# Optimization experiments

Measured on AMD Instinct MI355X. Metric: run time of the kernel, lower is better.

The kernel has to match this reference:

```python
import jax, jax.numpy as jnp
import numpy as np
from jax import lax

NB, HH, WW, C = 8, 64, 64, 192
G, K, DW_K, PA_K = 12, 3, 5, 3
GC, P = C // G, K * K
PAD, STRIDE, DIL = 1, 1, 1
OFFSET_SCALE = 1.0
LN_EPS = 1e-5


def _grid_sample(img, grid):
    # img: (B,Cc,H,W); grid: (B,L,P,2) xy in [-1,1]; bilinear, zeros padding, align_corners=False
    B, Cc, H, W = img.shape
    gx = (grid[..., 0] + 1.0) * (W * 0.5) - 0.5
    gy = (grid[..., 1] + 1.0) * (H * 0.5) - 0.5
    x0, y0 = jnp.floor(gx), jnp.floor(gy)

    def gather(xi, yi):
        valid = (xi >= 0) & (xi <= W - 1) & (yi >= 0) & (yi <= H - 1)
        xc = jnp.clip(xi, 0, W - 1).astype(jnp.int32)
        yc = jnp.clip(yi, 0, H - 1).astype(jnp.int32)
        v = jax.vmap(lambda im, y, x: im[:, y, x])(img, yc, xc)  # (B,Cc,L,P)
        return v * valid[:, None].astype(img.dtype)

    wx1, wy1 = gx - x0, gy - y0
    wx0, wy0 = 1.0 - wx1, 1.0 - wy1
    return (gather(x0, y0) * (wx0 * wy0)[:, None]
            + gather(x0 + 1.0, y0) * (wx1 * wy0)[:, None]
            + gather(x0, y0 + 1.0) * (wx0 * wy1)[:, None]
            + gather(x0 + 1.0, y0 + 1.0) * (wx1 * wy1)[:, None])


def _dcnv3_core(x, offset, mask):
    # x: (N,H,W,C) projected input; offset: (N,H,W,G*P*2); mask: (N,H,W,G*P)
    N, H, W, _ = x.shape
    xp = jnp.pad(x, ((0, 0), (PAD, PAD), (PAD, PAD), (0, 0)))
    Hp, Wp = H + 2 * PAD, W + 2 * PAD
    Ho, Wo = offset.shape[1], offset.shape[2]
    base = (DIL * (K - 1)) // 2 + 0.5
    ref_y = (base + jnp.arange(Ho) * STRIDE) / Hp
    ref_x = (base + jnp.arange(Wo) * STRIDE) / Wp
    ref = jnp.stack(jnp.broadcast_arrays(ref_x[None, :], ref_y[:, None]), -1)  # (Ho,Wo,2) xy
    start = -((DIL * (K - 1)) // 2)
    pts = (start + jnp.arange(K) * DIL).astype(x.dtype)
    gxg = jnp.broadcast_to((pts / Wp)[:, None], (K, K))  # w offset varies along dim0 (torch order)
    gyg = jnp.broadcast_to((pts / Hp)[None, :], (K, K))
    grid = jnp.tile(jnp.stack([gxg, gyg], -1).reshape(P, 2), (G, 1))  # (G*P,2)
    loc = ref[None, :, :, None, :] + grid * OFFSET_SCALE  # (1,Ho,Wo,G*P,2)
    norm = jnp.array([Wp, Hp], dtype=x.dtype)
    loc = loc + offset.reshape(N, Ho, Wo, G * P, 2) * OFFSET_SCALE / norm
    sg = 2.0 * loc - 1.0  # (N,Ho,Wo,G*P,2)
    img = xp.reshape(N, Hp * Wp, G, GC).transpose(0, 2, 3, 1).reshape(N * G, GC, Hp, Wp)
    grd = sg.reshape(N, Ho * Wo, G, P, 2).transpose(0, 2, 1, 3, 4).reshape(N * G, Ho * Wo, P, 2)
    samp = _grid_sample(img, grd)  # (N*G, GC, L, P)
    m = mask.reshape(N, Ho * Wo, G, P).transpose(0, 2, 1, 3).reshape(N * G, 1, Ho * Wo, P)
    out = (samp * m).sum(-1)  # (N*G, GC, L)
    return out.reshape(N, G, GC, Ho * Wo).transpose(0, 3, 1, 2).reshape(N, Ho, Wo, C)


def _dcnv3(x, dw_w, dw_b, ln_g, ln_b, off_w, off_b, msk_w, msk_b, in_w, in_b, out_w, out_b, cfs_w, cfs_b):
    N, H, W, _ = x.shape
    x_proj = x @ in_w + in_b
    # depthwise conv (5x5) -> LayerNorm (channels_last) -> GELU(exact)
    u = lax.conv_general_dilated(x, dw_w, (1, 1), 'SAME',
                                 dimension_numbers=('NHWC', 'HWIO', 'NHWC'),
                                 feature_group_count=C) + dw_b
    mu = u.mean(-1, keepdims=True)
    var = ((u - mu) ** 2).mean(-1, keepdims=True)
    u = (u - mu) * lax.rsqrt(var + LN_EPS) * ln_g + ln_b
    u = jax.nn.gelu(u, approximate=False)
    offset = u @ off_w + off_b  # (N,H,W,G*P*2)
    m = jax.nn.softmax((u @ msk_w + msk_b).reshape(N, H, W, G, P), axis=-1).reshape(N, H, W, G * P)
    y = _dcnv3_core(x_proj, offset, m)
    cfs = jax.nn.sigmoid(u @ cfs_w + cfs_b)  # (N,H,W,G)
    cfs = jnp.repeat(cfs, GC, axis=-1)       # (N,H,W,C), group-blockwise
    y = y * (1.0 - cfs) + x_proj * cfs
    return y @ out_w + out_b


def _patch_attention(x):
    # x: (N,H,W,C) -> std over softmax'd 3x3 neighbor scores: (N,H,W)
    N, H, W, _ = x.shape
    pad = (PA_K - 1) // 2
    xp = jnp.pad(x, ((0, 0), (pad, pad), (pad, pad), (0, 0)))
    neigh = jnp.stack([xp[:, i:i + H, j:j + W, :] for i in range(PA_K) for j in range(PA_K)],
                      axis=-1)  # (N,H,W,C,K1*K2), torch unfold ordering
    scores = jnp.einsum('nhwc,nhwck->nhwk', x, neigh)
    sm = jax.nn.softmax(scores, axis=-1)
    return jnp.std(sm, axis=-1, ddof=1)  # torch.std is unbiased


def setup_inputs() -> dict:
    key = jax.random.key(0)
    ks = jax.random.split(key, 8)
    s = 0.02
    return {
        'x': jax.random.normal(ks[0], (NB, HH, WW, C), jnp.float32),
        'dw_w': jax.random.normal(ks[1], (DW_K, DW_K, 1, C), jnp.float32) * s,
        'dw_b': jnp.zeros((C,), jnp.float32),
        'ln_g': jnp.ones((C,), jnp.float32),
        'ln_b': jnp.zeros((C,), jnp.float32),
        'off_w': jax.random.normal(ks[2], (C, G * P * 2), jnp.float32) * s,
        'off_b': jnp.zeros((G * P * 2,), jnp.float32),
        'msk_w': jax.random.normal(ks[3], (C, G * P), jnp.float32) * s,
        'msk_b': jnp.zeros((G * P,), jnp.float32),
        'in_w': jax.random.normal(ks[4], (C, C), jnp.float32) * s,
        'in_b': jnp.zeros((C,), jnp.float32),
        'out_w': jax.random.normal(ks[5], (C, C), jnp.float32) * s,
        'out_b': jnp.zeros((C,), jnp.float32),
        'cfs_w': jax.random.normal(ks[6], (C, G), jnp.float32) * s,
        'cfs_b': jnp.zeros((G,), jnp.float32),
    }


def reference(x, dw_w, dw_b, ln_g, ln_b, off_w, off_b, msk_w, msk_b, in_w, in_b, out_w, out_b, cfs_w, cfs_b):
    x1 = _dcnv3(x, dw_w, dw_b, ln_g, ln_b, off_w, off_b, msk_w, msk_b, in_w, in_b, out_w, out_b, cfs_w, cfs_b)
    mask = _patch_attention(x1)           # (N,H,W)
    return x + x1 * mask[..., None]
```

## Files before the change

### kernel.cpp

```cpp
#include <hip/hip_runtime.h>
#include <hip/hip_bf16.h>
#include <math.h>

#define NB 8
#define HH 64
#define WW 64
#define C 192
#define G 12
#define GC 16
#define P 9
#define NPIX (NB*HH*WW)

typedef __attribute__((ext_vector_type(8))) short short8;
typedef __attribute__((ext_vector_type(4))) float f32x4;
typedef unsigned short ushort;

__device__ __forceinline__ ushort to_bf16(float f) {
  __hip_bfloat16 b = __float2bfloat16(f);
  return *(ushort*)&b;
}
__device__ __forceinline__ float bf2f(ushort u) {
  union { unsigned u; float f; } cv; cv.u = ((unsigned)u) << 16; return cv.f;
}
__device__ __forceinline__ float bflo(unsigned u) {
  union { unsigned v; float f; } c; c.v = u << 16; return c.f;
}
__device__ __forceinline__ float bfhi(unsigned u) {
  union { unsigned v; float f; } c; c.v = u & 0xffff0000u; return c.f;
}

__global__ __launch_bounds__(256) void cvt_kernel(const float* __restrict__ in,
                                                  ushort* __restrict__ out) {
  int i = blockIdx.x*256 + threadIdx.x;
  float4 v0 = ((const float4*)in)[2*i];
  float4 v1 = ((const float4*)in)[2*i+1];
  short8 r;
  r[0]=to_bf16(v0.x); r[1]=to_bf16(v0.y); r[2]=to_bf16(v0.z); r[3]=to_bf16(v0.w);
  r[4]=to_bf16(v1.x); r[5]=to_bf16(v1.y); r[6]=to_bf16(v1.z); r[7]=to_bf16(v1.w);
  ((short8*)out)[i] = r;
}

__global__ void prep_w_kernel(const float* __restrict__ in_w, const float* __restrict__ out_w,
    const float* __restrict__ off_w, const float* __restrict__ msk_w, const float* __restrict__ cfs_w,
    const float* __restrict__ off_b, const float* __restrict__ msk_b, const float* __restrict__ cfs_b,
    ushort* __restrict__ in_wt, ushort* __restrict__ out_wt, ushort* __restrict__ wf_t,
    float* __restrict__ bf_bias) {
  int idx = blockIdx.x*256 + threadIdx.x;
  if (idx < 36864) {
    int n = idx/192, k = idx%192;
    in_wt[idx] = to_bf16(in_w[k*192 + n]);
  } else if (idx < 73728) {
    int j = idx - 36864; int n = j/192, k = j%192;
    out_wt[j] = to_bf16(out_w[k*192 + n]);
  } else if (idx < 147456) {
    int j = idx - 73728; int n = j/192, k = j%192;
    float v = 0.f;
    if (n < 216)      v = off_w[k*216 + n];
    else if (n < 324) v = msk_w[k*108 + (n-216)];
    else if (n < 336) v = cfs_w[k*12  + (n-324)];
    wf_t[j] = to_bf16(v);
  }
  if (idx < 384) {
    float b = 0.f;
    if (idx < 216)      b = off_b[idx];
    else if (idx < 324) b = msk_b[idx-216];
    else if (idx < 336) b = cfs_b[idx-324];
    bf_bias[idx] = b;
  }
}

template<int NW, int NSTORE, bool BF16OUT>
__global__ __launch_bounds__(256) void mfma_gemm(const ushort* __restrict__ A,
    const ushort* __restrict__ Wt, const float* __restrict__ bias,
    void* __restrict__ Cout_) {
  __shared__ ushort As[4*128*8];
  __shared__ ushort Bs[4*64*8];
  int pix0 = blockIdx.x * 128, n0 = blockIdx.y * 64;
  int tid = threadIdx.x;
  int wid = tid >> 6, lane = tid & 63;
  int lr = lane >> 4, lc = lane & 15;

  f32x4 acc[2][4];
  #pragma unroll
  for (int m=0;m<2;m++)
    #pragma unroll
    for (int j=0;j<4;j++) acc[m][j] = (f32x4){0.f,0.f,0.f,0.f};

  int sa0_kb = tid >> 7,        sa0_row = tid & 127;
  int sa1_kb = (tid+256) >> 7,  sa1_row = (tid+256) & 127;
  int sb_kb  = tid >> 6,        sb_n    = tid & 63;

  short8 pa0, pa1, pb;
  auto load_tile = [&](int k0) {
    pa0 = *(const short8*)&A[(size_t)(pix0 + sa0_row)*192 + k0 + sa0_kb*8];
    pa1 = *(const short8*)&A[(size_t)(pix0 + sa1_row)*192 + k0 + sa1_kb*8];
    pb  = *(const short8*)&Wt[(size_t)(n0 + sb_n)*192 + k0 + sb_kb*8];
  };
  load_tile(0);

  for (int t = 0; t < 6; t++) {
    __syncthreads();
    *(short8*)&As[(size_t)tid*8]        = pa0;
    *(short8*)&As[(size_t)(tid+256)*8]  = pa1;
    *(short8*)&Bs[(size_t)tid*8]        = pb;
    __syncthreads();
    if (t < 5) load_tile((t+1)*32);
    short8 a0 = *(const short8*)&As[(size_t)(lr*128 + wid*32 + lc)*8];
    short8 a1 = *(const short8*)&As[(size_t)(lr*128 + wid*32 + 16 + lc)*8];
    #pragma unroll
    for (int j=0;j<4;j++) {
      short8 b = *(const short8*)&Bs[(size_t)(lr*64 + j*16 + lc)*8];
      acc[0][j] = __builtin_amdgcn_mfma_f32_16x16x32_bf16(a0, b, acc[0][j], 0,0,0);
      acc[1][j] = __builtin_amdgcn_mfma_f32_16x16x32_bf16(a1, b, acc[1][j], 0,0,0);
    }
  }
  #pragma unroll
  for (int j=0;j<4;j++) {
    int col = n0 + j*16 + lc;
    if (NW != NSTORE && col >= NSTORE) continue;
    float bb = bias[col];
    #pragma unroll
    for (int m=0;m<2;m++) {
      size_t rbase = pix0 + wid*32 + m*16 + lr*4;
      #pragma unroll
      for (int r=0;r<4;r++) {
        float v = acc[m][j][r] + bb;
        if (BF16OUT) ((ushort*)Cout_)[(rbase + r)*NSTORE + col] = to_bf16(v);
        else         ((float*) Cout_)[(rbase + r)*NSTORE + col] = v;
      }
    }
  }
}

#define SEG 16
__global__ __launch_bounds__(192) void dw_ln_gelu_kernel(const float* __restrict__ x,
    const float* __restrict__ dw_w, const float* __restrict__ dw_b,
    const float* __restrict__ ln_g, const float* __restrict__ ln_b,
    ushort* __restrict__ u_out) {
  int blk = blockIdx.x;
  int qw = blk & 3; int nh = blk >> 2;
  int h = nh & 63, n = nh >> 6;
  int c = threadIdx.x;
  int w0 = qw * SEG;

  float kw[25];
  #pragma unroll
  for (int t=0;t<25;t++) kw[t] = dw_w[t*C + c];

  float acc[SEG];
  float bb = dw_b[c];
  #pragma unroll
  for (int i=0;i<SEG;i++) acc[i] = bb;

  #pragma unroll
  for (int i=0;i<5;i++) {
    int hy = h + i - 2;
    if (hy < 0 || hy >= HH) continue;
    const float* rowp = &x[(((size_t)n*HH + hy)*WW)*C + c];
    #pragma unroll
    for (int wi=0; wi<SEG+4; wi++) {
      int w_in = w0 - 2 + wi;
      if (w_in < 0 || w_in >= WW) continue;
      float v = rowp[(size_t)w_in*C];
      #pragma unroll
      for (int j=0;j<5;j++) {
        int a = wi - j;
        if (a >= 0 && a < SEG) acc[a] += v * kw[i*5+j];
      }
    }
  }

  __shared__ float lds_acc[SEG][C+1];
  __shared__ float part1[SEG][12], part2[SEG][12];
  __shared__ float mu_s[SEG], rs_s[SEG];
  #pragma unroll
  for (int i=0;i<SEG;i++) lds_acc[i][c] = acc[i];
  __syncthreads();
  {
    int p = threadIdx.x & 15, chunk = threadIdx.x >> 4;
    float s1 = 0.f, s2 = 0.f;
    #pragma unroll
    for (int k=0;k<16;k++) {
      float v = lds_acc[p][chunk*16 + k];
      s1 += v; s2 += v*v;
    }
    part1[p][chunk] = s1; part2[p][chunk] = s2;
  }
  __syncthreads();
  if (threadIdx.x < SEG) {
    int p = threadIdx.x;
    float t1 = 0.f, t2 = 0.f;
    #pragma unroll
    for (int k=0;k<12;k++){ t1 += part1[p][k]; t2 += part2[p][k]; }
    float mu = t1 * (1.0f/C);
    float var = t2 * (1.0f/C) - mu*mu;
    mu_s[p] = mu; rs_s[p] = rsqrtf(var + 1e-5f);
  }
  __syncthreads();
  float gg = ln_g[c], lb = ln_b[c];
  size_t obase = ((size_t)nh*WW + w0)*C + c;
  #pragma unroll
  for (int i=0;i<SEG;i++) {
    float uv = (acc[i] - mu_s[i])*rs_s[i]*gg + lb;
    uv = 0.5f*uv*(1.0f + erff(uv*0.70710678118654752f));
    u_out[obase + (size_t)i*C] = to_bf16(uv);
  }
}

#define SPX 4
__global__ __launch_bounds__(192) void sample_kernel(const float* __restrict__ omc,
    const ushort* __restrict__ x_proj, ushort* __restrict__ y_out) {
  int pix0 = blockIdx.x * SPX;
  int n = pix0 >> 12;
  int hw = pix0 & 4095; int h = hw >> 6; int w0 = hw & 63;
  int tid = threadIdx.x;
  __shared__ int   addrs[SPX*108*4];
  __shared__ float wts[SPX*108*4];
  __shared__ float msm[SPX][108];
  __shared__ float cfss[SPX][12];

  for (int i = tid; i < SPX*108; i += 192) {
    int px = i / 108, gp = i % 108;
    int p = gp % 9;
    const float pts[3] = {-1.f, 0.f, 1.f};
    float ox = omc[(size_t)(pix0+px)*336 + 2*gp];
    float oy = omc[(size_t)(pix0+px)*336 + 2*gp + 1];
    float gx = 1.0f + (float)(w0+px) + pts[p/3] + ox;
    float gy = 1.0f + (float)h + pts[p%3] + oy;
    float x0f = floorf(gx), y0f = floorf(gy);
    float wx1 = gx - x0f, wy1 = gy - y0f;
    float wx0 = 1.f-wx1, wy0 = 1.f-wy1;
    int x0 = (int)x0f, y0 = (int)y0f;
    bool xv0 = (x0   >= 1) && (x0   <= 64);
    bool xv1 = (x0+1 >= 1) && (x0+1 <= 64);
    bool yv0 = (y0   >= 1) && (y0   <= 64);
    bool yv1 = (y0+1 >= 1) && (y0+1 <= 64);
    int base = n*HH*WW*C;
    int4 a4;
    a4.x = (yv0&&xv0) ? (base + ((y0-1)*WW + (x0-1))*C)*2 : 0;
    a4.y = (yv0&&xv1) ? (base + ((y0-1)*WW + (x0  ))*C)*2 : 0;
    a4.z = (yv1&&xv0) ? (base + ((y0  )*WW + (x0-1))*C)*2 : 0;
    a4.w = (yv1&&xv1) ? (base + ((y0  )*WW + (x0  ))*C)*2 : 0;
    ((int4*)addrs)[i] = a4;
    float4 w4;
    w4.x = (yv0&&xv0) ? wx0*wy0 : 0.f;
    w4.y = (yv0&&xv1) ? wx1*wy0 : 0.f;
    w4.z = (yv1&&xv0) ? wx0*wy1 : 0.f;
    w4.w = (yv1&&xv1) ? wx1*wy1 : 0.f;
    ((float4*)wts)[i] = w4;
  }
  if (tid < SPX*12) {
    int px = tid / 12, gg = tid % 12;
    const float* mrow = &omc[(size_t)(pix0+px)*336 + 216 + gg*9];
    float m = -1e30f;
    #pragma unroll
    for (int p=0;p<P;p++) m = fmaxf(m, mrow[p]);
    float e[P]; float s = 0.f;
    #pragma unroll
    for (int p=0;p<P;p++){ e[p] = expf(mrow[p]-m); s += e[p]; }
    float inv = 1.0f/s;
    #pragma unroll
    for (int p=0;p<P;p++) msm[px][gg*9+p] = e[p]*inv;
  } else if (tid < SPX*12*2) {
    int q = tid - SPX*12;
    int px = q / 12, gg = q % 12;
    cfss[px][gg] = 1.0f/(1.0f+expf(-omc[(size_t)(pix0+px)*336 + 324 + gg]));
  }
  __syncthreads();
  for (int i = tid; i < SPX*108; i += 192) {
    int px = i / 108, gp = i % 108;
    float m = msm[px][gp] * (1.0f - cfss[px][gp/9]);
    f32x4 w4 = *(f32x4*)&wts[i*4];
    w4 *= m;
    *(f32x4*)&wts[i*4] = w4;
  }
  __syncthreads();
  int px = tid / 48, s = tid % 48;
  int g = s >> 2;
  int cb = s * 8;
  const char* xb = (const char*)x_proj;
  float4 accY = {0.f,0.f,0.f,0.f};
  #pragma unroll
  for (int p=0;p<P;p++){
    int gp = g*P + p;
    int4   a4 = ((const int4*)addrs)[px*108+gp];
    float4 w4 = ((const float4*)wts)[px*108+gp];
    uint2 q0 = *(const uint2*)(xb + (unsigned)(a4.x + cb));
    uint2 q1 = *(const uint2*)(xb + (unsigned)(a4.y + cb));
    uint2 q2 = *(const uint2*)(xb + (unsigned)(a4.z + cb));
    uint2 q3 = *(const uint2*)(xb + (unsigned)(a4.w + cb));
    accY.x += w4.x*bflo(q0.x) + w4.y*bflo(q1.x) + w4.z*bflo(q2.x) + w4.w*bflo(q3.x);
    accY.y += w4.x*bfhi(q0.x) + w4.y*bfhi(q1.x) + w4.z*bfhi(q2.x) + w4.w*bfhi(q3.x);
    accY.z += w4.x*bflo(q0.y) + w4.y*bflo(q1.y) + w4.z*bflo(q2.y) + w4.w*bflo(q3.y);
    accY.w += w4.x*bfhi(q0.y) + w4.y*bfhi(q1.y) + w4.z*bfhi(q2.y) + w4.w*bfhi(q3.y);
  }
  float cf = cfss[px][g];
  uint2 qx = *(const uint2*)(xb + ((size_t)(pix0+px)*C)*2 + cb);
  accY.x += bflo(qx.x)*cf;
  accY.y += bfhi(qx.x)*cf;
  accY.z += bflo(qx.y)*cf;
  accY.w += bfhi(qx.y)*cf;
  ushort4 r;
  r.x = to_bf16(accY.x); r.y = to_bf16(accY.y);
  r.z = to_bf16(accY.z); r.w = to_bf16(accY.w);
  *(ushort4*)&y_out[(size_t)(pix0+px)*C + s*4] = r;
}

__global__ __launch_bounds__(256) void pattn_kernel(const float* __restrict__ x,
    const ushort* __restrict__ x1, float* __restrict__ out) {
  int pix = blockIdx.x*4 + (threadIdx.x>>6);
  int lane = threadIdx.x & 63;
  int n = pix / (HH*WW); int hw = pix % (HH*WW); int h = hw / WW; int w = hw % WW;
  size_t base = (size_t)pix*C;
  float cen[3];
  #pragma unroll
  for (int q=0;q<3;q++) cen[q] = bf2f(x1[base + lane + 64*q]);
  float sc[9];
  #pragma unroll
  for (int i=0;i<3;i++){
    int hy = h+i-1;
    #pragma unroll
    for (int j=0;j<3;j++){
      int wx = w+j-1;
      float a = 0.f;
      if (hy>=0 && hy<HH && wx>=0 && wx<WW){
        size_t nb = ((size_t)(n*HH+hy)*WW + wx)*C;
        #pragma unroll
        for (int q=0;q<3;q++) a += cen[q]*bf2f(x1[nb + lane + 64*q]);
      }
      sc[i*3+j]=a;
    }
  }
  #pragma unroll
  for (int k=0;k<9;k++){
    #pragma unroll
    for (int o=32;o>0;o>>=1) sc[k] += __shfl_xor(sc[k], o);
  }
  float m = sc[0];
  #pragma unroll
  for (int k=1;k<9;k++) m = fmaxf(m, sc[k]);
  float pr[9]; float s = 0.f;
  #pragma unroll
  for (int k=0;k<9;k++){ pr[k] = expf(sc[k]-m); s += pr[k]; }
  float inv = 1.0f/s;
  float mean = 0.f;
  #pragma unroll
  for (int k=0;k<9;k++){ pr[k] *= inv; mean += pr[k]; }
  mean *= (1.0f/9.0f);
  float var = 0.f;
  #pragma unroll
  for (int k=0;k<9;k++){ float d = pr[k]-mean; var += d*d; }
  float sd = sqrtf(var*(1.0f/8.0f));
  #pragma unroll
  for (int q=0;q<3;q++){
    int c = lane + 64*q;
    out[base+c] = x[base+c] + bf2f(x1[base+c])*sd;
  }
}

extern "C" void kernel_launch(void* const* d_in, const int* in_sizes, int n_in,
                              void* d_out, int out_size, void* d_ws, size_t ws_size,
                              hipStream_t stream) {
  const float* x     = (const float*)d_in[0];
  const float* dw_w  = (const float*)d_in[1];
  const float* dw_b  = (const float*)d_in[2];
  const float* ln_g  = (const float*)d_in[3];
  const float* ln_b  = (const float*)d_in[4];
  const float* off_w = (const float*)d_in[5];
  const float* off_b = (const float*)d_in[6];
  const float* msk_w = (const float*)d_in[7];
  const float* msk_b = (const float*)d_in[8];
  const float* in_w  = (const float*)d_in[9];
  const float* in_b  = (const float*)d_in[10];
  const float* out_w = (const float*)d_in[11];
  const float* out_b = (const float*)d_in[12];
  const float* cfs_w = (const float*)d_in[13];
  const float* cfs_b = (const float*)d_in[14];
  float* outp = (float*)d_out;

  float*  omc    = (float*)d_ws;
  ushort* xproj  = (ushort*)(omc + (size_t)NPIX*336);
  ushort* x_bf   = xproj + (size_t)NPIX*192;
  ushort* u_bf   = x_bf + (size_t)NPIX*192;
  ushort* in_wt  = u_bf + (size_t)NPIX*192;
  ushort* out_wt = in_wt + 192*192;
  ushort* wf_t   = out_wt + 192*192;
  float*  bfb    = (float*)(wf_t + 384*192);

  cvt_kernel<<<NPIX*192/8/256, 256, 0, stream>>>(x, x_bf);
  prep_w_kernel<<<(147456+255)/256, 256, 0, stream>>>(in_w, out_w, off_w, msk_w, cfs_w,
                                                       off_b, msk_b, cfs_b,
                                                       in_wt, out_wt, wf_t, bfb);
  mfma_gemm<192,192,true><<<dim3(NPIX/128, 3), 256, 0, stream>>>(x_bf, in_wt, in_b, xproj);
  dw_ln_gelu_kernel<<<NB*HH*4, 192, 0, stream>>>(x, dw_w, dw_b, ln_g, ln_b, u_bf);
  mfma_gemm<384,336,false><<<dim3(NPIX/128, 6), 256, 0, stream>>>(u_bf, wf_t, bfb, omc);
  sample_kernel<<<NPIX/SPX, 192, 0, stream>>>(omc, xproj, u_bf);
  mfma_gemm<192,192,true><<<dim3(NPIX/128, 3), 256, 0, stream>>>(u_bf, out_wt, out_b, x_bf);
  pattn_kernel<<<NPIX/4, 256, 0, stream>>>(x, x_bf, outp);
}
```

Measured before the change: 157.8 us.

## Store offset/mask GEMM output in bf16, batch sample loads, tile patch attention in LDS

The offset/mask/cfs GEMM now writes bf16 instead of fp32, which halves the traffic written to and read from the omc buffer. The sample kernel reads those values as bf16 pairs and issues its bilinear gathers in batches of 12 to expose more memory-level parallelism. Patch attention is rewritten to load an 8x8 pixel tile plus halo into shared memory, split the dot products across 4 threads per pixel, and reduce through LDS. This replaces the repeated global neighbour reads and wave shuffles. Rounding the offsets and mask logits to bf16 loses precision in the sampling locations.

New measurement: 158.4 us. Within noise of the previous version (+0.3%).

```diff
diff --git a/kernel.cpp b/kernel.cpp
--- a/kernel.cpp
+++ b/kernel.cpp
@@ -208,7 +208,7 @@
 }
 
 #define SPX 4
-__global__ __launch_bounds__(192) void sample_kernel(const float* __restrict__ omc,
+__global__ __launch_bounds__(192) void sample_kernel(const ushort* __restrict__ omc,
     const ushort* __restrict__ x_proj, ushort* __restrict__ y_out) {
   int pix0 = blockIdx.x * SPX;
   int n = pix0 >> 12;
@@ -223,8 +223,8 @@
     int px = i / 108, gp = i % 108;
     int p = gp % 9;
     const float pts[3] = {-1.f, 0.f, 1.f};
-    float ox = omc[(size_t)(pix0+px)*336 + 2*gp];
-    float oy = omc[(size_t)(pix0+px)*336 + 2*gp + 1];
+    unsigned off2 = ((const unsigned*)omc)[(size_t)(pix0+px)*168 + gp];
+    float ox = bflo(off2), oy = bfhi(off2);
     float gx = 1.0f + (float)(w0+px) + pts[p/3] + ox;
     float gy = 1.0f + (float)h + pts[p%3] + oy;
     float x0f = floorf(gx), y0f = floorf(gy);
@@ -251,20 +251,23 @@
   }
   if (tid < SPX*12) {
     int px = tid / 12, gg = tid % 12;
-    const float* mrow = &omc[(size_t)(pix0+px)*336 + 216 + gg*9];
+    const ushort* mrow = &omc[(size_t)(pix0+px)*336 + 216 + gg*9];
+    float lv[P];
+    #pragma unroll
+    for (int p=0;p<P;p++) lv[p] = bf2f(mrow[p]);
     float m = -1e30f;
     #pragma unroll
-    for (int p=0;p<P;p++) m = fmaxf(m, mrow[p]);
+    for (int p=0;p<P;p++) m = fmaxf(m, lv[p]);
     float e[P]; float s = 0.f;
     #pragma unroll
-    for (int p=0;p<P;p++){ e[p] = expf(mrow[p]-m); s += e[p]; }
+    for (int p=0;p<P;p++){ e[p] = expf(lv[p]-m); s += e[p]; }
     float inv = 1.0f/s;
     #pragma unroll
     for (int p=0;p<P;p++) msm[px][gg*9+p] = e[p]*inv;
   } else if (tid < SPX*12*2) {
     int q = tid - SPX*12;
     int px = q / 12, gg = q % 12;
-    cfss[px][gg] = 1.0f/(1.0f+expf(-omc[(size_t)(pix0+px)*336 + 324 + gg]));
+    cfss[px][gg] = 1.0f/(1.0f+expf(-bf2f(omc[(size_t)(pix0+px)*336 + 324 + gg])));
   }
   __syncthreads();
   for (int i = tid; i < SPX*108; i += 192) {
@@ -275,24 +278,48 @@
     *(f32x4*)&wts[i*4] = w4;
   }
   __syncthreads();
-  int px = tid / 48, s = tid % 48;
+  int px = tid / 48, s = tid - (tid/48)*48;
   int g = s >> 2;
   int cb = s * 8;
   const char* xb = (const char*)x_proj;
   float4 accY = {0.f,0.f,0.f,0.f};
   #pragma unroll
-  for (int p=0;p<P;p++){
-    int gp = g*P + p;
-    int4   a4 = ((const int4*)addrs)[px*108+gp];
-    float4 w4 = ((const float4*)wts)[px*108+gp];
-    uint2 q0 = *(const uint2*)(xb + (unsigned)(a4.x + cb));
-    uint2 q1 = *(const uint2*)(xb + (unsigned)(a4.y + cb));
-    uint2 q2 = *(const uint2*)(xb + (unsigned)(a4.z + cb));
-    uint2 q3 = *(const uint2*)(xb + (unsigned)(a4.w + cb));
-    accY.x += w4.x*bflo(q0.x) + w4.y*bflo(q1.x) + w4.z*bflo(q2.x) + w4.w*bflo(q3.x);
-    accY.y += w4.x*bfhi(q0.x) + w4.y*bfhi(q1.x) + w4.z*bfhi(q2.x) + w4.w*bfhi(q3.x);
-    accY.z += w4.x*bflo(q0.y) + w4.y*bflo(q1.y) + w4.z*bflo(q2.y) + w4.w*bflo(q3.y);
-    accY.w += w4.x*bfhi(q0.y) + w4.y*bfhi(q1.y) + w4.z*bfhi(q2.y) + w4.w*bfhi(q3.y);
+  for (int pb = 0; pb < 3; pb++) {
+    uint2 q0_, q1_, q2_, q3_, q4_, q5_, q6_, q7_, q8_, q9_, qa_, qb_;
+    float4 wv0, wv1, wv2;
+    {
+      int gp = g*9 + pb*3;
+      int4 a0 = ((const int4*)addrs)[px*108+gp];
+      int4 a1 = ((const int4*)addrs)[px*108+gp+1];
+      int4 a2 = ((const int4*)addrs)[px*108+gp+2];
+      wv0 = ((const float4*)wts)[px*108+gp];
+      wv1 = ((const float4*)wts)[px*108+gp+1];
+      wv2 = ((const float4*)wts)[px*108+gp+2];
+      q0_ = *(const uint2*)(xb + (unsigned)(a0.x + cb));
+      q1_ = *(const uint2*)(xb + (unsigned)(a0.y + cb));
+      q2_ = *(const uint2*)(xb + (unsigned)(a0.z + cb));
+      q3_ = *(const uint2*)(xb + (unsigned)(a0.w + cb));
+      q4_ = *(const uint2*)(xb + (unsigned)(a1.x + cb));
+      q5_ = *(const uint2*)(xb + (unsigned)(a1.y + cb));
+      q6_ = *(const uint2*)(xb + (unsigned)(a1.z + cb));
+      q7_ = *(const uint2*)(xb + (unsigned)(a1.w + cb));
+      q8_ = *(const uint2*)(xb + (unsigned)(a2.x + cb));
+      q9_ = *(const uint2*)(xb + (unsigned)(a2.y + cb));
+      qa_ = *(const uint2*)(xb + (unsigned)(a2.z + cb));
+      qb_ = *(const uint2*)(xb + (unsigned)(a2.w + cb));
+    }
+    accY.x += wv0.x*bflo(q0_.x) + wv0.y*bflo(q1_.x) + wv0.z*bflo(q2_.x) + wv0.w*bflo(q3_.x);
+    accY.y += wv0.x*bfhi(q0_.x) + wv0.y*bfhi(q1_.x) + wv0.z*bfhi(q2_.x) + wv0.w*bfhi(q3_.x);
+    accY.z += wv0.x*bflo(q0_.y) + wv0.y*bflo(q1_.y) + wv0.z*bflo(q2_.y) + wv0.w*bflo(q3_.y);
+    accY.w += wv0.x*bfhi(q0_.y) + wv0.y*bfhi(q1_.y) + wv0.z*bfhi(q2_.y) + wv0.w*bfhi(q3_.y);
+    accY.x += wv1.x*bflo(q4_.x) + wv1.y*bflo(q5_.x) + wv1.z*bflo(q6_.x) + wv1.w*bflo(q7_.x);
+    accY.y += wv1.x*bfhi(q4_.x) + wv1.y*bfhi(q5_.x) + wv1.z*bfhi(q6_.x) + wv1.w*bfhi(q7_.x);
+    accY.z += wv1.x*bflo(q4_.y) + wv1.y*bflo(q5_.y) + wv1.z*bflo(q6_.y) + wv1.w*bflo(q7_.y);
+    accY.w += wv1.x*bfhi(q4_.y) + wv1.y*bfhi(q5_.y) + wv1.z*bfhi(q6_.y) + wv1.w*bfhi(q7_.y);
+    accY.x += wv2.x*bflo(q8_.x) + wv2.y*bflo(q9_.x) + wv2.z*bflo(qa_.x) + wv2.w*bflo(qb_.x);
+    accY.y += wv2.x*bfhi(q8_.x) + wv2.y*bfhi(q9_.x) + wv2.z*bfhi(qa_.x) + wv2.w*bfhi(qb_.x);
+    accY.z += wv2.x*bflo(q8_.y) + wv2.y*bflo(q9_.y) + wv2.z*bflo(qa_.y) + wv2.w*bflo(qb_.y);
+    accY.w += wv2.x*bfhi(q8_.y) + wv2.y*bfhi(q9_.y) + wv2.z*bfhi(qa_.y) + wv2.w*bfhi(qb_.y);
   }
   float cf = cfss[px][g];
   uint2 qx = *(const uint2*)(xb + ((size_t)(pix0+px)*C)*2 + cb);
@@ -308,53 +335,78 @@
 
 __global__ __launch_bounds__(256) void pattn_kernel(const float* __restrict__ x,
     const ushort* __restrict__ x1, float* __restrict__ out) {
-  int pix = blockIdx.x*4 + (threadIdx.x>>6);
-  int lane = threadIdx.x & 63;
-  int n = pix / (HH*WW); int hw = pix % (HH*WW); int h = hw / WW; int w = hw % WW;
-  size_t base = (size_t)pix*C;
-  float cen[3];
-  #pragma unroll
-  for (int q=0;q<3;q++) cen[q] = bf2f(x1[base + lane + 64*q]);
-  float sc[9];
-  #pragma unroll
-  for (int i=0;i<3;i++){
-    int hy = h+i-1;
-    #pragma unroll
-    for (int j=0;j<3;j++){
-      int wx = w+j-1;
+  __shared__ unsigned xs[100*97];
+  __shared__ float psc[64][36];
+  __shared__ float sd_s[64];
+  int blk = blockIdx.x;
+  int n = blk >> 6;
+  int ty = (blk >> 3) & 7, tx = blk & 7;
+  int th0 = ty*8, tw0 = tx*8;
+  int tid = threadIdx.x;
+  const unsigned* x1u = (const unsigned*)x1;
+  for (int i = tid; i < 100*96; i += 256) {
+    int cell = i / 96, wd = i - cell*96;
+    int gy = th0 - 1 + cell/10, gx = tw0 - 1 + cell%10;
+    unsigned v = 0;
+    if (gy>=0 && gy<HH && gx>=0 && gx<WW)
+      v = x1u[(((size_t)n*HH+gy)*WW+gx)*96 + wd];
+    xs[cell*97 + wd] = v;
+  }
+  __syncthreads();
+  {
+    int px = tid >> 2, qq = tid & 3;
+    int py = px >> 3, pxx = px & 7;
+    int cell = (py+1)*10 + (pxx+1);
+    float cen[48];
+    #pragma unroll
+    for (int k=0;k<24;k++) {
+      unsigned w = xs[cell*97 + qq*24 + k];
+      cen[2*k] = bflo(w); cen[2*k+1] = bfhi(w);
+    }
+    #pragma unroll
+    for (int ni=0;ni<9;ni++) {
+      int nc = cell + (ni/3-1)*10 + (ni%3-1);
       float a = 0.f;
-      if (hy>=0 && hy<HH && wx>=0 && wx<WW){
-        size_t nb = ((size_t)(n*HH+hy)*WW + wx)*C;
-        #pragma unroll
-        for (int q=0;q<3;q++) a += cen[q]*bf2f(x1[nb + lane + 64*q]);
+      #pragma unroll
+      for (int k=0;k<24;k++) {
+        unsigned w = xs[nc*97 + qq*24 + k];
+        a += cen[2*k]*bflo(w) + cen[2*k+1]*bfhi(w);
       }
-      sc[i*3+j]=a;
-    }
-  }
-  #pragma unroll
-  for (int k=0;k<9;k++){
-    #pragma unroll
-    for (int o=32;o>0;o>>=1) sc[k] += __shfl_xor(sc[k], o);
-  }
-  float m = sc[0];
-  #pragma unroll
-  for (int k=1;k<9;k++) m = fmaxf(m, sc[k]);
-  float pr[9]; float s = 0.f;
-  #pragma unroll
-  for (int k=0;k<9;k++){ pr[k] = expf(sc[k]-m); s += pr[k]; }
-  float inv = 1.0f/s;
-  float mean = 0.f;
-  #pragma unroll
-  for (int k=0;k<9;k++){ pr[k] *= inv; mean += pr[k]; }
-  mean *= (1.0f/9.0f);
-  float var = 0.f;
-  #pragma unroll
-  for (int k=0;k<9;k++){ float d = pr[k]-mean; var += d*d; }
-  float sd = sqrtf(var*(1.0f/8.0f));
-  #pragma unroll
-  for (int q=0;q<3;q++){
-    int c = lane + 64*q;
-    out[base+c] = x[base+c] + bf2f(x1[base+c])*sd;
+      psc[px][qq*9+ni] = a;
+    }
+  }
+  __syncthreads();
+  if (tid < 64) {
+    float sc[9];
+    #pragma unroll
+    for (int k=0;k<9;k++)
+      sc[k] = psc[tid][k] + psc[tid][9+k] + psc[tid][18+k] + psc[tid][27+k];
+    float m = sc[0];
+    #pragma unroll
+    for (int k=1;k<9;k++) m = fmaxf(m, sc[k]);
+    float pr[9]; float s = 0.f;
+    #pragma unroll
+    for (int k=0;k<9;k++){ pr[k] = expf(sc[k]-m); s += pr[k]; }
+    float inv = 1.0f/s;
+    float mean = 0.f;
+    #pragma unroll
+    for (int k=0;k<9;k++){ pr[k] *= inv; mean += pr[k]; }
+    mean *= (1.0f/9.0f);
+    float var = 0.f;
+    #pragma unroll
+    for (int k=0;k<9;k++){ float d = pr[k]-mean; var += d*d; }
+    sd_s[tid] = sqrtf(var*(1.0f/8.0f));
+  }
+  __syncthreads();
+  for (int i = tid; i < 64*96; i += 256) {
+    int p2 = i / 96, wd = i - p2*96;
+    int py2 = p2 >> 3, px2 = p2 & 7;
+    unsigned v = xs[((py2+1)*10 + (px2+1))*97 + wd];
+    size_t pix = ((size_t)n*HH + th0+py2)*WW + tw0+px2;
+    float2 xv = ((const float2*)x)[pix*96 + wd];
+    float sd = sd_s[p2];
+    float2 o; o.x = xv.x + bflo(v)*sd; o.y = xv.y + bfhi(v)*sd;
+    ((float2*)out)[pix*96 + wd] = o;
   }
 }
 
@@ -378,8 +430,8 @@
   const float* cfs_b = (const float*)d_in[14];
   float* outp = (float*)d_out;
 
-  float*  omc    = (float*)d_ws;
-  ushort* xproj  = (ushort*)(omc + (size_t)NPIX*336);
+  ushort* omc    = (ushort*)d_ws;
+  ushort* xproj  = omc + (size_t)NPIX*336;
   ushort* x_bf   = xproj + (size_t)NPIX*192;
   ushort* u_bf   = x_bf + (size_t)NPIX*192;
   ushort* in_wt  = u_bf + (size_t)NPIX*192;
@@ -393,8 +445,8 @@
                                                        in_wt, out_wt, wf_t, bfb);
   mfma_gemm<192,192,true><<<dim3(NPIX/128, 3), 256, 0, stream>>>(x_bf, in_wt, in_b, xproj);
   dw_ln_gelu_kernel<<<NB*HH*4, 192, 0, stream>>>(x, dw_w, dw_b, ln_g, ln_b, u_bf);
-  mfma_gemm<384,336,false><<<dim3(NPIX/128, 6), 256, 0, stream>>>(u_bf, wf_t, bfb, omc);
+  mfma_gemm<384,336,true><<<dim3(NPIX/128, 6), 256, 0, stream>>>(u_bf, wf_t, bfb, omc);
   sample_kernel<<<NPIX/SPX, 192, 0, stream>>>(omc, xproj, u_bf);
   mfma_gemm<192,192,true><<<dim3(NPIX/128, 3), 256, 0, stream>>>(u_bf, out_wt, out_b, x_bf);
-  pattn_kernel<<<NPIX/4, 256, 0, stream>>>(x, x_bf, outp);
-}
+  pattn_kernel<<<NB*64, 256, 0, stream>>>(x, x_bf, outp);
+}
```
